# Kernel optimization log

Measured on AMD Instinct MI355X. Metric: run time of the kernel, lower is better.

## Reference

```python
import jax, jax.numpy as jnp
import numpy as np

B, T, C, V = 8, 2048, 1024, 32000


def setup_inputs() -> dict:
    key = jax.random.key(0)
    ks = jax.random.split(key, 12)
    s = 1.0 / np.sqrt(C)
    return {
        "input_tokens": jax.random.randint(ks[0], (B, T), 0, V),
        "xx_init": jnp.zeros((B, C), jnp.float32),
        "aa_init": jnp.zeros((B, C), jnp.float32),
        "bb_init": jnp.zeros((B, C), jnp.float32),
        "pp_init": jnp.zeros((B, C), jnp.float32),  # with aa=bb=0 this is equivalent to -inf init
        "emb": jax.random.normal(ks[1], (V, C), jnp.float32) * 0.02,
        "time_mix_k": jax.random.uniform(ks[2], (C,), jnp.float32),
        "time_mix_v": jax.random.uniform(ks[3], (C,), jnp.float32),
        "time_mix_r": jax.random.uniform(ks[4], (C,), jnp.float32),
        "time_decay": jax.random.normal(ks[5], (C,), jnp.float32) * 0.1,
        "time_first": jax.random.normal(ks[6], (C,), jnp.float32) * 0.1,
        "Wk": jax.random.normal(ks[7], (C, C), jnp.float32) * s,
        "Wv": jax.random.normal(ks[8], (C, C), jnp.float32) * s,
        "Wr": jax.random.normal(ks[9], (C, C), jnp.float32) * s,
        "Wo": jax.random.normal(ks[10], (C, C), jnp.float32) * s,
    }


def _wkv_scan(k, v, aa0, bb0, pp0, w, u):
    """Numerically-stable RWKV WKV recurrence.
    k, v: [T, B, C]; aa0/bb0/pp0: [B, C]; w (decay, negative), u (bonus): [C]."""
    def step(carry, kv):
        aa, bb, pp = carry
        kt, vt = kv
        ww = u + kt
        p = jnp.maximum(pp, ww)
        e1 = jnp.exp(pp - p)
        e2 = jnp.exp(ww - p)
        wkv = (e1 * aa + e2 * vt) / (e1 * bb + e2)
        ww2 = pp + w
        p2 = jnp.maximum(ww2, kt)
        e1b = jnp.exp(ww2 - p2)
        e2b = jnp.exp(kt - p2)
        return (e1b * aa + e2b * vt, e1b * bb + e2b, p2), wkv
    (aa, bb, pp), out = jax.lax.scan(step, (aa0, bb0, pp0), (k, v))
    return out, aa, bb, pp


def _forward(input_tokens, xx_init, aa_init, bb_init, pp_init, emb,
             time_mix_k, time_mix_v, time_mix_r, time_decay, time_first,
             Wk, Wv, Wr, Wo):
    x = emb[input_tokens]                                   # [B, T, C]
    xprev = jnp.concatenate([xx_init[:, None, :], x[:, :-1]], axis=1)  # token shift
    xk = x * time_mix_k + xprev * (1.0 - time_mix_k)
    xv = x * time_mix_v + xprev * (1.0 - time_mix_v)
    xr = x * time_mix_r + xprev * (1.0 - time_mix_r)
    k = jnp.einsum("btc,dc->btd", xk, Wk)
    v = jnp.einsum("btc,dc->btd", xv, Wv)
    r = jax.nn.sigmoid(jnp.einsum("btc,dc->btd", xr, Wr))
    w = -jnp.exp(time_decay)                                # per-channel decay
    u = time_first
    wkv, _, _, _ = _wkv_scan(jnp.swapaxes(k, 0, 1), jnp.swapaxes(v, 0, 1),
                             aa_init, bb_init, pp_init, w, u)
    wkv = jnp.swapaxes(wkv, 0, 1)                           # [B, T, C]
    rwkv = jnp.einsum("btc,dc->btd", r * wkv, Wo)
    e1 = rwkv[:, -1]          # final-step state
    e2 = rwkv.mean(axis=1)    # time-averaged state
    hx = (e1 + e2) * 0.5
    return jnp.stack([hx, hx])  # (hx, cx) stacked -> [2, B, C]


def reference(input_tokens, xx_init, aa_init, bb_init, pp_init, emb,
              time_mix_k, time_mix_v, time_mix_r, time_decay, time_first,
              Wk, Wv, Wr, Wo):
    return _forward(input_tokens, xx_init, aa_init, bb_init, pp_init, emb,
                    time_mix_k, time_mix_v, time_mix_r, time_decay, time_first,
                    Wk, Wv, Wr, Wo)
```

## Files before the change

kernel.cpp:

```cpp
#include <hip/hip_runtime.h>

#define Bdim 8
#define Tdim 2048
#define Cdim 1024
#define CHUNK 16
#define NCHUNK 128
#define BC (Bdim*Cdim)

typedef float floatx4 __attribute__((ext_vector_type(4)));
typedef _Float16 half8 __attribute__((ext_vector_type(8)));
typedef _Float16 half4v __attribute__((ext_vector_type(4)));

__device__ __forceinline__ void load16(const void* g, void* l) {
    __builtin_amdgcn_global_load_lds(
        (const __attribute__((address_space(1))) void*)g,
        (__attribute__((address_space(3))) void*)l, 16, 0, 0);
}

__global__ __launch_bounds__(256) void embed_mix3(const int* __restrict__ tokens,
                                                  const float* __restrict__ xx_init,
                                                  const float* __restrict__ emb,
                                                  const float* __restrict__ tmk,
                                                  const float* __restrict__ tmv,
                                                  const float* __restrict__ tmr,
                                                  _Float16* __restrict__ xk,
                                                  _Float16* __restrict__ xv,
                                                  _Float16* __restrict__ xr) {
    int row = blockIdx.x;
    int b = row >> 11;
    int t = row & (Tdim - 1);
    const float* cur = emb + (size_t)tokens[row] * Cdim;
    const float* prv = (t == 0) ? (xx_init + (size_t)b * Cdim)
                                : (emb + (size_t)tokens[row - 1] * Cdim);
    int c = threadIdx.x * 4;
    float4 cf4 = *reinterpret_cast<const float4*>(cur + c);
    float4 pf4 = *reinterpret_cast<const float4*>(prv + c);
    float4 mk = *reinterpret_cast<const float4*>(tmk + c);
    float4 mv = *reinterpret_cast<const float4*>(tmv + c);
    float4 mr = *reinterpret_cast<const float4*>(tmr + c);
    float cf[4] = {cf4.x, cf4.y, cf4.z, cf4.w};
    float pf[4] = {pf4.x, pf4.y, pf4.z, pf4.w};
    float mkf[4] = {mk.x, mk.y, mk.z, mk.w};
    float mvf[4] = {mv.x, mv.y, mv.z, mv.w};
    float mrf[4] = {mr.x, mr.y, mr.z, mr.w};
    half4v hk, hv, hr;
    #pragma unroll
    for (int j = 0; j < 4; j++) {
        hk[j] = (_Float16)(mkf[j] * cf[j] + (1.0f - mkf[j]) * pf[j]);
        hv[j] = (_Float16)(mvf[j] * cf[j] + (1.0f - mvf[j]) * pf[j]);
        hr[j] = (_Float16)(mrf[j] * cf[j] + (1.0f - mrf[j]) * pf[j]);
    }
    size_t o = (size_t)row * Cdim + c;
    *reinterpret_cast<half4v*>(xk + o) = hk;
    *reinterpret_cast<half4v*>(xv + o) = hv;
    *reinterpret_cast<half4v*>(xr + o) = hr;
}

__global__ __launch_bounds__(256) void wconv(const float* __restrict__ Wk,
                                             const float* __restrict__ Wv,
                                             const float* __restrict__ Wr,
                                             _Float16* __restrict__ Wh) {
    const float* W = blockIdx.y == 0 ? Wk : (blockIdx.y == 1 ? Wv : Wr);
    _Float16* dst = Wh + (size_t)blockIdx.y * Cdim * Cdim;
    int i = (blockIdx.x * 256 + threadIdx.x) * 4;
    float4 f = *reinterpret_cast<const float4*>(W + i);
    half4v h;
    h[0] = (_Float16)f.x; h[1] = (_Float16)f.y; h[2] = (_Float16)f.z; h[3] = (_Float16)f.w;
    *reinterpret_cast<half4v*>(dst + i) = h;
}

__global__ __launch_bounds__(256) void gemm_kvr(const _Float16* __restrict__ xk,
                                                const _Float16* __restrict__ xv,
                                                const _Float16* __restrict__ xr,
                                                const _Float16* __restrict__ Wh,
                                                _Float16* __restrict__ ko,
                                                _Float16* __restrict__ vo,
                                                _Float16* __restrict__ ro) {
    const int which = blockIdx.y;
    const _Float16* X = which == 0 ? xk : (which == 1 ? xv : xr);
    const _Float16* W = Wh + (size_t)which * Cdim * Cdim;
    _Float16* out     = which == 0 ? ko : (which == 1 ? vo : ro);

    const int lin = blockIdx.x;
    const int xcd = lin & 7;
    const int loc = lin >> 3;
    const int mt = xcd * 16 + (loc >> 3);
    const int nt = loc & 7;
    const int m0 = mt * 128;
    const int n0 = nt * 128;

    __shared__ _Float16 As[128 * 64];
    __shared__ _Float16 Bs[128 * 64];

    const int tid = threadIdx.x;
    const int lane = tid & 63;
    const int wave = tid >> 6;
    const int wm = (wave >> 1) * 64;
    const int wn = (wave & 1) * 64;
    const int lr = lane & 15;
    const int lk = lane >> 4;

    const _Float16* Asrc = X + (size_t)m0 * Cdim;
    const _Float16* Bsrc = W + (size_t)n0 * Cdim;

    floatx4 acc[4][4] = {};

    for (int k0 = 0; k0 < Cdim; k0 += 64) {
        #pragma unroll
        for (int i = 0; i < 4; i++) {
            int e = i * 256 + tid;
            int r = e >> 3;
            int cbp = e & 7;
            int cbl = cbp ^ (r & 7);
            load16(Asrc + (size_t)r * Cdim + k0 + cbl * 8, (char*)As + e * 16);
            load16(Bsrc + (size_t)r * Cdim + k0 + cbl * 8, (char*)Bs + e * 16);
        }
        __syncthreads();
        #pragma unroll
        for (int kk = 0; kk < 64; kk += 32) {
            const int kb_ = kk >> 3;
            half8 af[4], bf[4];
            #pragma unroll
            for (int mi = 0; mi < 4; mi++) {
                int r = wm + mi * 16 + lr;
                int cb = (kb_ + lk) ^ (r & 7);
                af[mi] = *reinterpret_cast<const half8*>(As + r * 64 + cb * 8);
            }
            #pragma unroll
            for (int ni = 0; ni < 4; ni++) {
                int r = wn + ni * 16 + lr;
                int cb = (kb_ + lk) ^ (r & 7);
                bf[ni] = *reinterpret_cast<const half8*>(Bs + r * 64 + cb * 8);
            }
            #pragma unroll
            for (int mi = 0; mi < 4; mi++)
                #pragma unroll
                for (int ni = 0; ni < 4; ni++)
                    acc[mi][ni] = __builtin_amdgcn_mfma_f32_16x16x32_f16(af[mi], bf[ni], acc[mi][ni], 0, 0, 0);
        }
        __syncthreads();
    }

    #pragma unroll
    for (int mi = 0; mi < 4; mi++) {
        #pragma unroll
        for (int ni = 0; ni < 4; ni++) {
            #pragma unroll
            for (int reg = 0; reg < 4; reg++) {
                int mm = m0 + wm + mi * 16 + (lane >> 4) * 4 + reg;
                int nn = n0 + wn + ni * 16 + (lane & 15);
                float v = acc[mi][ni][reg];
                if (which == 2) v = 1.0f / (1.0f + __expf(-v));
                out[(size_t)mm * Cdim + nn] = (_Float16)v;
            }
        }
    }
}

__global__ __launch_bounds__(256) void scan_pass1(const _Float16* __restrict__ kb,
                                                  const _Float16* __restrict__ vb,
                                                  const float* __restrict__ tdecay,
                                                  float* __restrict__ tot_a,
                                                  float* __restrict__ tot_b,
                                                  float* __restrict__ tot_p) {
    int g = blockIdx.x * 256 + threadIdx.x;
    int j = g >> 10;
    int rem = g & 1023;
    int b = rem >> 7;
    int c8 = (rem & 127) << 3;
    float4 td0 = *reinterpret_cast<const float4*>(tdecay + c8);
    float4 td1 = *reinterpret_cast<const float4*>(tdecay + c8 + 4);
    float w[8] = {-__expf(td0.x), -__expf(td0.y), -__expf(td0.z), -__expf(td0.w),
                  -__expf(td1.x), -__expf(td1.y), -__expf(td1.z), -__expf(td1.w)};
    float aa[8], bb[8], pp[8];
    #pragma unroll
    for (int i = 0; i < 8; i++) { aa[i] = 0.0f; bb[i] = 0.0f; pp[i] = -1e30f; }
    const size_t base = ((size_t)(b * Tdim + j * CHUNK)) * Cdim + c8;
    const _Float16* kp = kb + base;
    const _Float16* vp = vb + base;
    #pragma unroll 4
    for (int t = 0; t < CHUNK; t++) {
        half8 k8 = *reinterpret_cast<const half8*>(kp + (size_t)t * Cdim);
        half8 v8 = *reinterpret_cast<const half8*>(vp + (size_t)t * Cdim);
        #pragma unroll
        for (int i = 0; i < 8; i++) {
            float kt = (float)k8[i];
            float vt = (float)v8[i];
            float ww2 = pp[i] + w[i];
            float p2 = fmaxf(ww2, kt);
            float e1 = __expf(ww2 - p2);
            float e2 = __expf(kt - p2);
            aa[i] = e1 * aa[i] + e2 * vt;
            bb[i] = e1 * bb[i] + e2;
            pp[i] = p2;
        }
    }
    size_t o = (size_t)j * BC + ((size_t)rem << 3);
    #pragma unroll
    for (int i = 0; i < 8; i++) {
        tot_a[o + i] = aa[i]; tot_b[o + i] = bb[i]; tot_p[o + i] = pp[i];
    }
}

__global__ __launch_bounds__(256) void combine_chunks(const float* __restrict__ tot_a,
                                                      const float* __restrict__ tot_b,
                                                      const float* __restrict__ tot_p,
                                                      const float* __restrict__ aa_init,
                                                      const float* __restrict__ bb_init,
                                                      const float* __restrict__ pp_init,
                                                      const float* __restrict__ tdecay,
                                                      float* __restrict__ inc_a,
                                                      float* __restrict__ inc_b,
                                                      float* __restrict__ inc_p) {
    int idx = blockIdx.x * 256 + threadIdx.x;
    int c = idx & (Cdim - 1);
    float w = -__expf(tdecay[c]);
    float wL = w * (float)CHUNK;
    float a = aa_init[idx], b = bb_init[idx], p = pp_init[idx];
    #pragma unroll 8
    for (int j = 0; j < NCHUNK; j++) {
        inc_a[j * BC + idx] = a;
        inc_b[j * BC + idx] = b;
        inc_p[j * BC + idx] = p;
        float ta = tot_a[j * BC + idx];
        float tb = tot_b[j * BC + idx];
        float tp = tot_p[j * BC + idx];
        float px = p + wL;
        float q = fmaxf(px, tp);
        float e1 = __expf(px - q);
        float e2 = __expf(tp - q);
        a = e1 * a + e2 * ta;
        b = e1 * b + e2 * tb;
        p = q;
    }
}

__global__ __launch_bounds__(256) void scan_pass2(const _Float16* __restrict__ kb,
                                                  const _Float16* __restrict__ vb,
                                                  const _Float16* __restrict__ rb,
                                                  const float* __restrict__ tdecay,
                                                  const float* __restrict__ tfirst,
                                                  const float* __restrict__ inc_a,
                                                  const float* __restrict__ inc_b,
                                                  const float* __restrict__ inc_p,
                                                  float* __restrict__ partial,
                                                  float* __restrict__ ylast) {
    int g = blockIdx.x * 256 + threadIdx.x;
    int j = g >> 10;
    int rem = g & 1023;
    int b = rem >> 7;
    int c8 = (rem & 127) << 3;
    float4 td0 = *reinterpret_cast<const float4*>(tdecay + c8);
    float4 td1 = *reinterpret_cast<const float4*>(tdecay + c8 + 4);
    float4 u0 = *reinterpret_cast<const float4*>(tfirst + c8);
    float4 u1 = *reinterpret_cast<const float4*>(tfirst + c8 + 4);
    float w[8] = {-__expf(td0.x), -__expf(td0.y), -__expf(td0.z), -__expf(td0.w),
                  -__expf(td1.x), -__expf(td1.y), -__expf(td1.z), -__expf(td1.w)};
    float u[8] = {u0.x, u0.y, u0.z, u0.w, u1.x, u1.y, u1.z, u1.w};
    size_t so = (size_t)j * BC + ((size_t)rem << 3);
    float aa[8], bb[8], pp[8], sum[8], ylv[8];
    #pragma unroll
    for (int i = 0; i < 8; i++) {
        aa[i] = inc_a[so + i]; bb[i] = inc_b[so + i]; pp[i] = inc_p[so + i];
        sum[i] = 0.0f; ylv[i] = 0.0f;
    }
    const size_t base = ((size_t)(b * Tdim + j * CHUNK)) * Cdim + c8;
    const _Float16* kp = kb + base;
    const _Float16* vp = vb + base;
    const _Float16* rp = rb + base;
    #pragma unroll 4
    for (int t = 0; t < CHUNK; t++) {
        half8 k8 = *reinterpret_cast<const half8*>(kp + (size_t)t * Cdim);
        half8 v8 = *reinterpret_cast<const half8*>(vp + (size_t)t * Cdim);
        half8 r8 = *reinterpret_cast<const half8*>(rp + (size_t)t * Cdim);
        #pragma unroll
        for (int i = 0; i < 8; i++) {
            float kt = (float)k8[i];
            float vt = (float)v8[i];
            float rt = (float)r8[i];
            float ww = u[i] + kt;
            float p = fmaxf(pp[i], ww);
            float e1 = __expf(pp[i] - p);
            float e2 = __expf(ww - p);
            float wkv = (e1 * aa[i] + e2 * vt) / (e1 * bb[i] + e2);
            float y = rt * wkv;
            sum[i] += y;
            ylv[i] = y;
            float ww2 = pp[i] + w[i];
            float p2 = fmaxf(ww2, kt);
            float e1b = __expf(ww2 - p2);
            float e2b = __expf(kt - p2);
            aa[i] = e1b * aa[i] + e2b * vt;
            bb[i] = e1b * bb[i] + e2b;
            pp[i] = p2;
        }
    }
    #pragma unroll
    for (int i = 0; i < 8; i++) partial[so + i] = sum[i];
    if (j == NCHUNK - 1) {
        size_t bo = ((size_t)rem << 3);
        #pragma unroll
        for (int i = 0; i < 8; i++) ylast[bo + i] = ylv[i];
    }
}

__global__ __launch_bounds__(256) void reduce_z(const float* __restrict__ partial,
                                                const float* __restrict__ ylast,
                                                float* __restrict__ z) {
    int idx = blockIdx.x * 256 + threadIdx.x;
    float s = 0.0f;
    #pragma unroll 8
    for (int j = 0; j < NCHUNK; j++) s += partial[j * BC + idx];
    z[idx] = 0.5f * (ylast[idx] + s * (1.0f / (float)Tdim));
}

__global__ __launch_bounds__(256) void final_out(const float* __restrict__ z,
                                                 const float* __restrict__ Wo,
                                                 float* __restrict__ out) {
    int gw = (blockIdx.x * 256 + threadIdx.x) >> 6;
    int lane = threadIdx.x & 63;
    int b = gw >> 10;
    int d = gw & (Cdim - 1);
    const float4* zr = reinterpret_cast<const float4*>(z + (size_t)b * Cdim);
    const float4* wr = reinterpret_cast<const float4*>(Wo + (size_t)d * Cdim);
    float acc = 0.0f;
    #pragma unroll
    for (int s = 0; s < 4; s++) {
        float4 a = zr[lane + 64 * s];
        float4 w4 = wr[lane + 64 * s];
        acc += a.x * w4.x + a.y * w4.y + a.z * w4.z + a.w * w4.w;
    }
    #pragma unroll
    for (int off = 32; off > 0; off >>= 1) acc += __shfl_down(acc, off);
    if (lane == 0) {
        out[(size_t)b * Cdim + d] = acc;
        out[(size_t)BC + (size_t)b * Cdim + d] = acc;
    }
}

extern "C" void kernel_launch(void* const* d_in, const int* in_sizes, int n_in,
                              void* d_out, int out_size, void* d_ws, size_t ws_size,
                              hipStream_t stream) {
    const int*   tokens  = (const int*)d_in[0];
    const float* xx_init = (const float*)d_in[1];
    const float* aa_init = (const float*)d_in[2];
    const float* bb_init = (const float*)d_in[3];
    const float* pp_init = (const float*)d_in[4];
    const float* emb     = (const float*)d_in[5];
    const float* tmk     = (const float*)d_in[6];
    const float* tmv     = (const float*)d_in[7];
    const float* tmr     = (const float*)d_in[8];
    const float* tdecay  = (const float*)d_in[9];
    const float* tfirst  = (const float*)d_in[10];
    const float* Wk      = (const float*)d_in[11];
    const float* Wv      = (const float*)d_in[12];
    const float* Wr      = (const float*)d_in[13];
    const float* Wo      = (const float*)d_in[14];
    float* out = (float*)d_out;

    char* ws = (char*)d_ws;
    size_t off = 0;
    auto alloc = [&](size_t bytes) -> void* {
        void* p = ws + off;
        off += (bytes + 255) & ~(size_t)255;
        return p;
    };
    _Float16* xkb = (_Float16*)alloc((size_t)Bdim * Tdim * Cdim * 2);
    _Float16* xvb = (_Float16*)alloc((size_t)Bdim * Tdim * Cdim * 2);
    _Float16* xrb = (_Float16*)alloc((size_t)Bdim * Tdim * Cdim * 2);
    _Float16* kb = (_Float16*)alloc((size_t)Bdim * Tdim * Cdim * 2);
    _Float16* vb = (_Float16*)alloc((size_t)Bdim * Tdim * Cdim * 2);
    _Float16* rb = (_Float16*)alloc((size_t)Bdim * Tdim * Cdim * 2);
    _Float16* Wh = (_Float16*)alloc((size_t)3 * Cdim * Cdim * 2);
    float* tot_a = (float*)alloc((size_t)NCHUNK * BC * 4);
    float* tot_b = (float*)alloc((size_t)NCHUNK * BC * 4);
    float* tot_p = (float*)alloc((size_t)NCHUNK * BC * 4);
    float* inc_a = (float*)alloc((size_t)NCHUNK * BC * 4);
    float* inc_b = (float*)alloc((size_t)NCHUNK * BC * 4);
    float* inc_p = (float*)alloc((size_t)NCHUNK * BC * 4);
    float* partial = (float*)alloc((size_t)NCHUNK * BC * 4);
    float* ylast   = (float*)alloc((size_t)BC * 4);
    float* zbuf    = (float*)alloc((size_t)BC * 4);

    embed_mix3<<<Bdim * Tdim, 256, 0, stream>>>(tokens, xx_init, emb, tmk, tmv, tmr,
                                                xkb, xvb, xrb);
    wconv<<<dim3(1024, 3), 256, 0, stream>>>(Wk, Wv, Wr, Wh);
    gemm_kvr<<<dim3(1024, 3), 256, 0, stream>>>(xkb, xvb, xrb, Wh, kb, vb, rb);
    scan_pass1<<<(NCHUNK * BC / 8) / 256, 256, 0, stream>>>(kb, vb, tdecay, tot_a, tot_b, tot_p);
    combine_chunks<<<BC / 256, 256, 0, stream>>>(tot_a, tot_b, tot_p, aa_init, bb_init, pp_init,
                                                 tdecay, inc_a, inc_b, inc_p);
    scan_pass2<<<(NCHUNK * BC / 8) / 256, 256, 0, stream>>>(kb, vb, rb, tdecay, tfirst,
                                                            inc_a, inc_b, inc_p, partial, ylast);
    reduce_z<<<BC / 256, 256, 0, stream>>>(partial, ylast, zbuf);
    final_out<<<(BC / 4), 256, 0, stream>>>(zbuf, Wo, out);
}
```

Measured before the change: 454.9 us.

## Fuse chunked WKV scan passes, combine and reduction into one LDS kernel

```diff
diff --git a/kernel.cpp b/kernel.cpp
--- a/kernel.cpp
+++ b/kernel.cpp
@@ -3,8 +3,9 @@
 #define Bdim 8
 #define Tdim 2048
 #define Cdim 1024
-#define CHUNK 16
-#define NCHUNK 128
+#define NCH 128
+#define CLEN 16
+#define CG 32
 #define BC (Bdim*Cdim)
 
 typedef float floatx4 __attribute__((ext_vector_type(4)));
@@ -157,35 +158,50 @@
     }
 }
 
-__global__ __launch_bounds__(256) void scan_pass1(const _Float16* __restrict__ kb,
+__global__ __launch_bounds__(1024) void wkv_fused(const _Float16* __restrict__ kb,
                                                   const _Float16* __restrict__ vb,
+                                                  const _Float16* __restrict__ rb,
                                                   const float* __restrict__ tdecay,
-                                                  float* __restrict__ tot_a,
-                                                  float* __restrict__ tot_b,
-                                                  float* __restrict__ tot_p) {
-    int g = blockIdx.x * 256 + threadIdx.x;
-    int j = g >> 10;
-    int rem = g & 1023;
-    int b = rem >> 7;
-    int c8 = (rem & 127) << 3;
-    float4 td0 = *reinterpret_cast<const float4*>(tdecay + c8);
-    float4 td1 = *reinterpret_cast<const float4*>(tdecay + c8 + 4);
-    float w[8] = {-__expf(td0.x), -__expf(td0.y), -__expf(td0.z), -__expf(td0.w),
-                  -__expf(td1.x), -__expf(td1.y), -__expf(td1.z), -__expf(td1.w)};
-    float aa[8], bb[8], pp[8];
-    #pragma unroll
-    for (int i = 0; i < 8; i++) { aa[i] = 0.0f; bb[i] = 0.0f; pp[i] = -1e30f; }
-    const size_t base = ((size_t)(b * Tdim + j * CHUNK)) * Cdim + c8;
+                                                  const float* __restrict__ tfirst,
+                                                  const float* __restrict__ aa_init,
+                                                  const float* __restrict__ bb_init,
+                                                  const float* __restrict__ pp_init,
+                                                  float* __restrict__ z) {
+    __shared__ float sa[NCH * CG];
+    __shared__ float sbv[NCH * CG];
+    __shared__ float sp[NCH * CG];
+    __shared__ float ssum[NCH * CG];
+    __shared__ float s2[8 * CG];
+    __shared__ float syl[CG];
+
+    const int b = blockIdx.x >> 5;
+    const int cg = blockIdx.x & 31;
+    const int tid = threadIdx.x;
+    const int cl = tid & 7;
+    const int j = tid >> 3;
+    const int c0 = cg * CG + cl * 4;
+
+    float4 td = *reinterpret_cast<const float4*>(tdecay + c0);
+    float4 u4 = *reinterpret_cast<const float4*>(tfirst + c0);
+    float w[4] = {-__expf(td.x), -__expf(td.y), -__expf(td.z), -__expf(td.w)};
+    float u[4] = {u4.x, u4.y, u4.z, u4.w};
+
+    const size_t base = ((size_t)(b * Tdim + j * CLEN)) * Cdim + c0;
     const _Float16* kp = kb + base;
     const _Float16* vp = vb + base;
+    const _Float16* rp = rb + base;
+
+    float aa[4], bb[4], pp[4];
+    #pragma unroll
+    for (int i = 0; i < 4; i++) { aa[i] = 0.0f; bb[i] = 0.0f; pp[i] = -1e30f; }
     #pragma unroll 4
-    for (int t = 0; t < CHUNK; t++) {
-        half8 k8 = *reinterpret_cast<const half8*>(kp + (size_t)t * Cdim);
-        half8 v8 = *reinterpret_cast<const half8*>(vp + (size_t)t * Cdim);
-        #pragma unroll
-        for (int i = 0; i < 8; i++) {
-            float kt = (float)k8[i];
-            float vt = (float)v8[i];
+    for (int t = 0; t < CLEN; t++) {
+        half4v k4 = *reinterpret_cast<const half4v*>(kp + (size_t)t * Cdim);
+        half4v v4 = *reinterpret_cast<const half4v*>(vp + (size_t)t * Cdim);
+        #pragma unroll
+        for (int i = 0; i < 4; i++) {
+            float kt = (float)k4[i];
+            float vt = (float)v4[i];
             float ww2 = pp[i] + w[i];
             float p2 = fmaxf(ww2, kt);
             float e1 = __expf(ww2 - p2);
@@ -195,89 +211,53 @@
             pp[i] = p2;
         }
     }
-    size_t o = (size_t)j * BC + ((size_t)rem << 3);
-    #pragma unroll
-    for (int i = 0; i < 8; i++) {
-        tot_a[o + i] = aa[i]; tot_b[o + i] = bb[i]; tot_p[o + i] = pp[i];
-    }
-}
-
-__global__ __launch_bounds__(256) void combine_chunks(const float* __restrict__ tot_a,
-                                                      const float* __restrict__ tot_b,
-                                                      const float* __restrict__ tot_p,
-                                                      const float* __restrict__ aa_init,
-                                                      const float* __restrict__ bb_init,
-                                                      const float* __restrict__ pp_init,
-                                                      const float* __restrict__ tdecay,
-                                                      float* __restrict__ inc_a,
-                                                      float* __restrict__ inc_b,
-                                                      float* __restrict__ inc_p) {
-    int idx = blockIdx.x * 256 + threadIdx.x;
-    int c = idx & (Cdim - 1);
-    float w = -__expf(tdecay[c]);
-    float wL = w * (float)CHUNK;
-    float a = aa_init[idx], b = bb_init[idx], p = pp_init[idx];
-    #pragma unroll 8
-    for (int j = 0; j < NCHUNK; j++) {
-        inc_a[j * BC + idx] = a;
-        inc_b[j * BC + idx] = b;
-        inc_p[j * BC + idx] = p;
-        float ta = tot_a[j * BC + idx];
-        float tb = tot_b[j * BC + idx];
-        float tp = tot_p[j * BC + idx];
-        float px = p + wL;
-        float q = fmaxf(px, tp);
-        float e1 = __expf(px - q);
-        float e2 = __expf(tp - q);
-        a = e1 * a + e2 * ta;
-        b = e1 * b + e2 * tb;
-        p = q;
-    }
-}
-
-__global__ __launch_bounds__(256) void scan_pass2(const _Float16* __restrict__ kb,
-                                                  const _Float16* __restrict__ vb,
-                                                  const _Float16* __restrict__ rb,
-                                                  const float* __restrict__ tdecay,
-                                                  const float* __restrict__ tfirst,
-                                                  const float* __restrict__ inc_a,
-                                                  const float* __restrict__ inc_b,
-                                                  const float* __restrict__ inc_p,
-                                                  float* __restrict__ partial,
-                                                  float* __restrict__ ylast) {
-    int g = blockIdx.x * 256 + threadIdx.x;
-    int j = g >> 10;
-    int rem = g & 1023;
-    int b = rem >> 7;
-    int c8 = (rem & 127) << 3;
-    float4 td0 = *reinterpret_cast<const float4*>(tdecay + c8);
-    float4 td1 = *reinterpret_cast<const float4*>(tdecay + c8 + 4);
-    float4 u0 = *reinterpret_cast<const float4*>(tfirst + c8);
-    float4 u1 = *reinterpret_cast<const float4*>(tfirst + c8 + 4);
-    float w[8] = {-__expf(td0.x), -__expf(td0.y), -__expf(td0.z), -__expf(td0.w),
-                  -__expf(td1.x), -__expf(td1.y), -__expf(td1.z), -__expf(td1.w)};
-    float u[8] = {u0.x, u0.y, u0.z, u0.w, u1.x, u1.y, u1.z, u1.w};
-    size_t so = (size_t)j * BC + ((size_t)rem << 3);
-    float aa[8], bb[8], pp[8], sum[8], ylv[8];
-    #pragma unroll
-    for (int i = 0; i < 8; i++) {
-        aa[i] = inc_a[so + i]; bb[i] = inc_b[so + i]; pp[i] = inc_p[so + i];
-        sum[i] = 0.0f; ylv[i] = 0.0f;
-    }
-    const size_t base = ((size_t)(b * Tdim + j * CHUNK)) * Cdim + c8;
-    const _Float16* kp = kb + base;
-    const _Float16* vp = vb + base;
-    const _Float16* rp = rb + base;
+    {
+        int o = j * CG + cl * 4;
+        #pragma unroll
+        for (int i = 0; i < 4; i++) { sa[o + i] = aa[i]; sbv[o + i] = bb[i]; sp[o + i] = pp[i]; }
+    }
+    __syncthreads();
+
+    if (tid < CG) {
+        int ch = tid;
+        float w1 = -__expf(tdecay[cg * CG + ch]);
+        float wL = w1 * (float)CLEN;
+        int gidx = b * Cdim + cg * CG + ch;
+        float a = aa_init[gidx], bbv = bb_init[gidx], p = pp_init[gidx];
+        for (int jj = 0; jj < NCH; jj++) {
+            int o = jj * CG + ch;
+            float ta = sa[o], tb = sbv[o], tp = sp[o];
+            sa[o] = a; sbv[o] = bbv; sp[o] = p;
+            float px = p + wL;
+            float q = fmaxf(px, tp);
+            float e1 = __expf(px - q);
+            float e2 = __expf(tp - q);
+            a = e1 * a + e2 * ta;
+            bbv = e1 * bbv + e2 * tb;
+            p = q;
+        }
+    }
+    __syncthreads();
+
+    float sum[4], ylv[4];
+    {
+        int o = j * CG + cl * 4;
+        #pragma unroll
+        for (int i = 0; i < 4; i++) {
+            aa[i] = sa[o + i]; bb[i] = sbv[o + i]; pp[i] = sp[o + i];
+            sum[i] = 0.0f; ylv[i] = 0.0f;
+        }
+    }
     #pragma unroll 4
-    for (int t = 0; t < CHUNK; t++) {
-        half8 k8 = *reinterpret_cast<const half8*>(kp + (size_t)t * Cdim);
-        half8 v8 = *reinterpret_cast<const half8*>(vp + (size_t)t * Cdim);
-        half8 r8 = *reinterpret_cast<const half8*>(rp + (size_t)t * Cdim);
-        #pragma unroll
-        for (int i = 0; i < 8; i++) {
-            float kt = (float)k8[i];
-            float vt = (float)v8[i];
-            float rt = (float)r8[i];
+    for (int t = 0; t < CLEN; t++) {
+        half4v k4 = *reinterpret_cast<const half4v*>(kp + (size_t)t * Cdim);
+        half4v v4 = *reinterpret_cast<const half4v*>(vp + (size_t)t * Cdim);
+        half4v r4 = *reinterpret_cast<const half4v*>(rp + (size_t)t * Cdim);
+        #pragma unroll
+        for (int i = 0; i < 4; i++) {
+            float kt = (float)k4[i];
+            float vt = (float)v4[i];
+            float rt = (float)r4[i];
             float ww = u[i] + kt;
             float p = fmaxf(pp[i], ww);
             float e1 = __expf(pp[i] - p);
@@ -295,23 +275,31 @@
             pp[i] = p2;
         }
     }
-    #pragma unroll
-    for (int i = 0; i < 8; i++) partial[so + i] = sum[i];
-    if (j == NCHUNK - 1) {
-        size_t bo = ((size_t)rem << 3);
-        #pragma unroll
-        for (int i = 0; i < 8; i++) ylast[bo + i] = ylv[i];
-    }
-}
-
-__global__ __launch_bounds__(256) void reduce_z(const float* __restrict__ partial,
-                                                const float* __restrict__ ylast,
-                                                float* __restrict__ z) {
-    int idx = blockIdx.x * 256 + threadIdx.x;
-    float s = 0.0f;
-    #pragma unroll 8
-    for (int j = 0; j < NCHUNK; j++) s += partial[j * BC + idx];
-    z[idx] = 0.5f * (ylast[idx] + s * (1.0f / (float)Tdim));
+    {
+        int o = j * CG + cl * 4;
+        #pragma unroll
+        for (int i = 0; i < 4; i++) ssum[o + i] = sum[i];
+        if (j == NCH - 1) {
+            #pragma unroll
+            for (int i = 0; i < 4; i++) syl[cl * 4 + i] = ylv[i];
+        }
+    }
+    __syncthreads();
+
+    if (tid < 256) {
+        int ch = tid & 31, s = tid >> 5;
+        float acc = 0.0f;
+        #pragma unroll
+        for (int jj = 0; jj < 16; jj++) acc += ssum[(s * 16 + jj) * CG + ch];
+        s2[s * CG + ch] = acc;
+    }
+    __syncthreads();
+    if (tid < CG) {
+        float acc = 0.0f;
+        #pragma unroll
+        for (int s = 0; s < 8; s++) acc += s2[s * CG + tid];
+        z[(size_t)b * Cdim + cg * CG + tid] = 0.5f * (syl[tid] + acc * (1.0f / (float)Tdim));
+    }
 }
 
 __global__ __launch_bounds__(256) void final_out(const float* __restrict__ z,
@@ -372,25 +360,13 @@
     _Float16* vb = (_Float16*)alloc((size_t)Bdim * Tdim * Cdim * 2);
     _Float16* rb = (_Float16*)alloc((size_t)Bdim * Tdim * Cdim * 2);
     _Float16* Wh = (_Float16*)alloc((size_t)3 * Cdim * Cdim * 2);
-    float* tot_a = (float*)alloc((size_t)NCHUNK * BC * 4);
-    float* tot_b = (float*)alloc((size_t)NCHUNK * BC * 4);
-    float* tot_p = (float*)alloc((size_t)NCHUNK * BC * 4);
-    float* inc_a = (float*)alloc((size_t)NCHUNK * BC * 4);
-    float* inc_b = (float*)alloc((size_t)NCHUNK * BC * 4);
-    float* inc_p = (float*)alloc((size_t)NCHUNK * BC * 4);
-    float* partial = (float*)alloc((size_t)NCHUNK * BC * 4);
-    float* ylast   = (float*)alloc((size_t)BC * 4);
-    float* zbuf    = (float*)alloc((size_t)BC * 4);
+    float* zbuf = (float*)alloc((size_t)BC * 4);
 
     embed_mix3<<<Bdim * Tdim, 256, 0, stream>>>(tokens, xx_init, emb, tmk, tmv, tmr,
                                                 xkb, xvb, xrb);
     wconv<<<dim3(1024, 3), 256, 0, stream>>>(Wk, Wv, Wr, Wh);
     gemm_kvr<<<dim3(1024, 3), 256, 0, stream>>>(xkb, xvb, xrb, Wh, kb, vb, rb);
-    scan_pass1<<<(NCHUNK * BC / 8) / 256, 256, 0, stream>>>(kb, vb, tdecay, tot_a, tot_b, tot_p);
-    combine_chunks<<<BC / 256, 256, 0, stream>>>(tot_a, tot_b, tot_p, aa_init, bb_init, pp_init,
-                                                 tdecay, inc_a, inc_b, inc_p);
-    scan_pass2<<<(NCHUNK * BC / 8) / 256, 256, 0, stream>>>(kb, vb, rb, tdecay, tfirst,
-                                                            inc_a, inc_b, inc_p, partial, ylast);
-    reduce_z<<<BC / 256, 256, 0, stream>>>(partial, ylast, zbuf);
+    wkv_fused<<<Bdim * 32, 1024, 0, stream>>>(kb, vb, rb, tdecay, tfirst,
+                                              aa_init, bb_init, pp_init, zbuf);
     final_out<<<(BC / 4), 256, 0, stream>>>(zbuf, Wo, out);
 }
```

Result: faster. 430.1 us (-5.5%).
